# Kernel optimization log

Measured on AMD Instinct MI355X. Metric: run time of the kernel, lower is better.

Reference implementation:

```python
import jax, jax.numpy as jnp
import numpy as np

D_MODEL = 1024
NUM_HEADS = 16


def setup_inputs() -> dict:
    key = jax.random.key(0)
    ks = jax.random.split(key, 5)
    scale = 1.0 / np.sqrt(D_MODEL)
    X = jax.random.normal(ks[0], (4, 2048, D_MODEL), dtype=jnp.float32)
    W_q = jax.random.normal(ks[1], (D_MODEL, D_MODEL), dtype=jnp.float32) * scale
    W_k = jax.random.normal(ks[2], (D_MODEL, D_MODEL), dtype=jnp.float32) * scale
    W_v = jax.random.normal(ks[3], (D_MODEL, D_MODEL), dtype=jnp.float32) * scale
    W_o = jax.random.normal(ks[4], (D_MODEL, D_MODEL), dtype=jnp.float32) * scale
    return {"X": X, "W_q": W_q, "W_k": W_k, "W_v": W_v, "W_o": W_o}


def reference(X, W_q, W_k, W_v, W_o):
    b, s, d_model = X.shape
    h = NUM_HEADS
    d_k = d_model // h
    # Linear projections (y = x @ W^T convention; W stored as [out,in] would be
    # x @ W.T, but with random weights we use x @ W — math is identical in form).
    def split_heads(y):
        return y.reshape(b, s, h, d_k).transpose(0, 2, 1, 3)  # b h s d
    q = split_heads(X @ W_q)
    k = split_heads(X @ W_k)
    v = split_heads(X @ W_v)
    scores = jnp.einsum('bhid,bhjd->bhij', q, k) / jnp.sqrt(jnp.float32(d_k))
    causal = jnp.tril(jnp.ones((s, s), dtype=bool))
    scores = jnp.where(causal[None, None], scores, jnp.float32(-jnp.inf))
    probs = jax.nn.softmax(scores, axis=-1)
    attended = jnp.einsum('bhij,bhjd->bhid', probs, v)
    out = attended.transpose(0, 2, 1, 3).reshape(b, s, d_model)
    return out @ W_o
```

## Files before the change

kernel.cpp:

```cpp
#include <hip/hip_runtime.h>

typedef __bf16 bf16;
typedef __attribute__((ext_vector_type(8))) __bf16 bf16x8;
typedef __attribute__((ext_vector_type(4))) float f32x4;
typedef __attribute__((ext_vector_type(16))) float f32x16;
typedef __attribute__((ext_vector_type(4))) unsigned short u16x4;
typedef __attribute__((ext_vector_type(2))) int v2i;

#define D_MODEL 1024
#define SEQ     2048
#define NB      4
#define NH      16
#define DK      64
#define MROWS   (NB * SEQ)

#define MFMA_BF16 __builtin_amdgcn_mfma_f32_16x16x32_bf16
#define MFMA32    __builtin_amdgcn_mfma_f32_32x32x16_bf16
#define EXP2F(x) __builtin_amdgcn_exp2f(x)
#define QSCALE 0.18033688011112042f

__device__ __forceinline__ bf16 f2b(float f) {
    union { float f; unsigned u; } c; c.f = f;
    unsigned r = (c.u + 0x7fffu + ((c.u >> 16) & 1u)) >> 16;
    union { unsigned short s; bf16 b; } o; o.s = (unsigned short)r;
    return o.b;
}
__device__ __forceinline__ unsigned short f2u(float f) {
    union { float f; unsigned u; } c; c.f = f;
    return (unsigned short)((c.u + 0x7fffu + ((c.u >> 16) & 1u)) >> 16);
}

__device__ __forceinline__ f32x16 zero16() {
    f32x16 z = {0.f,0.f,0.f,0.f,0.f,0.f,0.f,0.f,
                0.f,0.f,0.f,0.f,0.f,0.f,0.f,0.f};
    return z;
}

template <int N> struct IC { static constexpr int v = N; };

__global__ void prep_kernel(const float* __restrict__ X,
                            const float* __restrict__ Wq, const float* __restrict__ Wk,
                            const float* __restrict__ Wv, const float* __restrict__ Wo,
                            bf16* __restrict__ Xb, bf16* __restrict__ WqkvT,
                            bf16* __restrict__ WoT) {
    __shared__ float tile[32][33];
    const int bid = blockIdx.x;
    if (bid < 8192) {
        int i = bid * 256 + threadIdx.x;
        float4 v = ((const float4*)X)[i];
        u16x4 o; o[0] = f2u(v.x); o[1] = f2u(v.y); o[2] = f2u(v.z); o[3] = f2u(v.w);
        ((u16x4*)Xb)[i] = o;
    } else {
        int r = bid - 8192;
        int w = r >> 10, tl = r & 1023;
        const float* src = (w == 0) ? Wq : (w == 1) ? Wk : (w == 2) ? Wv : Wo;
        bf16* dst = (w == 3) ? WoT : WqkvT + (size_t)w * 1024 * 1024;
        const int n0 = (tl & 31) * 32, k0 = (tl >> 5) * 32;
        const int tx = threadIdx.x & 31, ty = threadIdx.x >> 5;
#pragma unroll
        for (int i = 0; i < 4; i++)
            tile[ty + i * 8][tx] = src[(size_t)(k0 + ty + i * 8) * 1024 + n0 + tx];
        __syncthreads();
#pragma unroll
        for (int i = 0; i < 4; i++)
            dst[(size_t)(n0 + ty + i * 8) * 1024 + k0 + tx] = f2b(tile[tx][ty + i * 8]);
    }
}

__global__ __launch_bounds__(256) void gemm_qkv(const bf16* __restrict__ A,
                                                const bf16* __restrict__ Bt,
                                                bf16* __restrict__ outQ,
                                                bf16* __restrict__ outV) {
    __shared__ __align__(16) bf16 lA[128 * 64];
    __shared__ __align__(16) bf16 lB[128 * 64];

    const int t = threadIdx.x;
    const int wid = t >> 6, lane = t & 63;
    const int ln = lane & 15, qd = lane >> 4;
    const int wm = wid >> 1, wn = wid & 1;

    const int bid = blockIdx.x;
    const int idx = bid >> 3;
    const int colb = (bid & 7) * 3 + (idx % 3);
    const int rowb = idx / 3;
    const int row0 = rowb * 128, col0 = colb * 128;
    const bool isQK = (col0 < 2048);

    const int srow = t >> 3;
    const int schunk = (t & 7) ^ (srow & 7);
    const bf16* ga = A  + (size_t)(row0 + srow) * 1024 + schunk * 8;
    const bf16* gb = Bt + (size_t)(col0 + srow) * 1024 + schunk * 8;
    const int swk = ln & 7;

    f32x4 acc[4][4];
#pragma unroll
    for (int i = 0; i < 4; i++)
#pragma unroll
        for (int j = 0; j < 4; j++) acc[i][j] = (f32x4){0.f, 0.f, 0.f, 0.f};

    for (int kb = 0; kb < 1024; kb += 64) {
#pragma unroll
        for (int c = 0; c < 4; c++) {
            __builtin_amdgcn_global_load_lds(
                (const __attribute__((address_space(1))) void*)(ga + kb + (size_t)c * 32 * 1024),
                (__attribute__((address_space(3))) void*)(&lA[t * 8 + c * 2048]), 16, 0, 0);
            __builtin_amdgcn_global_load_lds(
                (const __attribute__((address_space(1))) void*)(gb + kb + (size_t)c * 32 * 1024),
                (__attribute__((address_space(3))) void*)(&lB[t * 8 + c * 2048]), 16, 0, 0);
        }
        __syncthreads();

#pragma unroll
        for (int ks = 0; ks < 2; ks++) {
            bf16x8 af[4], bfr[4];
#pragma unroll
            for (int i = 0; i < 4; i++)
                af[i] = *(const bf16x8*)&lA[(wm * 64 + i * 16 + ln) * 64
                                            + ((ks * 4 + qd) ^ swk) * 8];
#pragma unroll
            for (int j = 0; j < 4; j++)
                bfr[j] = *(const bf16x8*)&lB[(wn * 64 + j * 16 + ln) * 64
                                             + ((ks * 4 + qd) ^ swk) * 8];
            if (isQK) {
#pragma unroll
                for (int i = 0; i < 4; i++)
#pragma unroll
                    for (int j = 0; j < 4; j++)
                        acc[i][j] = MFMA_BF16(bfr[j], af[i], acc[i][j], 0, 0, 0);
            } else {
#pragma unroll
                for (int i = 0; i < 4; i++)
#pragma unroll
                    for (int j = 0; j < 4; j++)
                        acc[i][j] = MFMA_BF16(af[i], bfr[j], acc[i][j], 0, 0, 0);
            }
        }
        __syncthreads();
    }

    if (isQK) {
#pragma unroll
        for (int i = 0; i < 4; i++)
#pragma unroll
            for (int j = 0; j < 4; j++) {
                int m  = row0 + wm * 64 + i * 16 + ln;
                int n0 = col0 + wn * 64 + j * 16 + qd * 4;
                float scale = (n0 < 1024) ? QSCALE : 1.0f;
                int b = m >> 11, s = m & 2047;
                int h = (n0 & 1023) >> 6, d0 = n0 & 63;
                size_t addr = (((size_t)(b * NH + h) * SEQ + s) * DK + d0)
                              + (size_t)(n0 >> 10) * 8388608;
                u16x4 w;
#pragma unroll
                for (int r = 0; r < 4; r++) w[r] = f2u(acc[i][j][r] * scale);
                *(u16x4*)&outQ[addr] = w;
            }
    } else {
#pragma unroll
        for (int i = 0; i < 4; i++)
#pragma unroll
            for (int j = 0; j < 4; j++) {
                int m0 = row0 + wm * 64 + i * 16 + qd * 4;
                int n  = col0 + wn * 64 + j * 16 + ln - 2048;
                int b = m0 >> 11, s0 = m0 & 2047;
                int h = n >> 6, d = n & 63;
                size_t addr = ((size_t)(b * NH + h) * DK + d) * SEQ + s0;
                u16x4 w;
#pragma unroll
                for (int r = 0; r < 4; r++) w[r] = f2u(acc[i][j][r]);
                *(u16x4*)&outV[addr] = w;
            }
    }
}

__global__ __launch_bounds__(256) void gemm_o(const bf16* __restrict__ A,
                                              const bf16* __restrict__ Bt,
                                              float* __restrict__ out) {
    __shared__ __align__(16) bf16 lA[128 * 64];
    __shared__ __align__(16) bf16 lB[128 * 64];

    const int t = threadIdx.x;
    const int wid = t >> 6, lane = t & 63;
    const int ln = lane & 15, qd = lane >> 4;
    const int wm = wid >> 1, wn = wid & 1;

    const int bid = blockIdx.x;
    const int colb = bid & 7, rowb = bid >> 3;
    const int row0 = rowb * 128, col0 = colb * 128;

    const int srow = t >> 3;
    const int schunk = (t & 7) ^ (srow & 7);
    const bf16* ga = A  + (size_t)(row0 + srow) * 1024 + schunk * 8;
    const bf16* gb = Bt + (size_t)(col0 + srow) * 1024 + schunk * 8;
    const int swk = ln & 7;

    f32x4 acc[4][4];
#pragma unroll
    for (int i = 0; i < 4; i++)
#pragma unroll
        for (int j = 0; j < 4; j++) acc[i][j] = (f32x4){0.f, 0.f, 0.f, 0.f};

    for (int kb = 0; kb < 1024; kb += 64) {
#pragma unroll
        for (int c = 0; c < 4; c++) {
            __builtin_amdgcn_global_load_lds(
                (const __attribute__((address_space(1))) void*)(ga + kb + (size_t)c * 32 * 1024),
                (__attribute__((address_space(3))) void*)(&lA[t * 8 + c * 2048]), 16, 0, 0);
            __builtin_amdgcn_global_load_lds(
                (const __attribute__((address_space(1))) void*)(gb + kb + (size_t)c * 32 * 1024),
                (__attribute__((address_space(3))) void*)(&lB[t * 8 + c * 2048]), 16, 0, 0);
        }
        __syncthreads();

#pragma unroll
        for (int ks = 0; ks < 2; ks++) {
            bf16x8 af[4], bfr[4];
#pragma unroll
            for (int i = 0; i < 4; i++)
                af[i] = *(const bf16x8*)&lA[(wm * 64 + i * 16 + ln) * 64
                                            + ((ks * 4 + qd) ^ swk) * 8];
#pragma unroll
            for (int j = 0; j < 4; j++)
                bfr[j] = *(const bf16x8*)&lB[(wn * 64 + j * 16 + ln) * 64
                                             + ((ks * 4 + qd) ^ swk) * 8];
#pragma unroll
            for (int i = 0; i < 4; i++)
#pragma unroll
                for (int j = 0; j < 4; j++)
                    acc[i][j] = MFMA_BF16(bfr[j], af[i], acc[i][j], 0, 0, 0);
        }
        __syncthreads();
    }

#pragma unroll
    for (int i = 0; i < 4; i++)
#pragma unroll
        for (int j = 0; j < 4; j++) {
            int m  = row0 + wm * 64 + i * 16 + ln;
            int n0 = col0 + wn * 64 + j * 16 + qd * 4;
            *(f32x4*)&out[(size_t)m * 1024 + n0] = acc[i][j];
        }
}

__global__ __launch_bounds__(256, 3) void attn_kernel(const bf16* __restrict__ Q,
                                                      const bf16* __restrict__ K,
                                                      const bf16* __restrict__ Vt,
                                                      bf16* __restrict__ attn_out) {
    __shared__ __align__(16) bf16 smem[4][64 * 64];

    const int t = threadIdx.x;
    const int wid = t >> 6, lane = t & 63;
    const int qcol = lane & 31, h = lane >> 5;

    const int bid = blockIdx.x;
    const int bh = ((bid >> 7) << 3) | (bid & 7);
    const int g  = 15 - ((bid >> 3) & 15);
    const int nsteps = 2 * g + 2;

    const bf16* Qh = Q  + (size_t)bh * SEQ * DK;
    const bf16* Kh = K  + (size_t)bh * SEQ * DK;
    const bf16* Vh = Vt + (size_t)bh * DK * SEQ;

    const int qw0 = g * 128 + wid * 32;

    const int srow = t >> 3;
    const int schunk = (t & 7) ^ (srow & 7);
    const bf16* kgp = Kh + (size_t)srow * DK + schunk * 8;
    const bf16* vgp = Vh + (size_t)srow * SEQ + schunk * 8;

    const char* sbase = (const char*)&smem[0][0];
    int raddr[4];
#pragma unroll
    for (int tt = 0; tt < 4; tt++)
        raddr[tt] = qcol * 128 + (((2 * tt + h) ^ (lane & 7)) * 16);

    bf16x8 qf[4];
#pragma unroll
    for (int tt = 0; tt < 4; tt++)
        qf[tt] = *(const bf16x8*)(Qh + (size_t)(qw0 + qcol) * DK + tt * 16 + h * 8);

    f32x16 o[2];
    o[0] = zero16(); o[1] = zero16();
    float l = 0.f;

    auto stage = [&](int kb, int buf) {
#pragma unroll
        for (int c = 0; c < 2; c++) {
            __builtin_amdgcn_global_load_lds(
                (const __attribute__((address_space(1))) void*)(kgp + (size_t)(kb + c * 32) * DK),
                (__attribute__((address_space(3))) void*)(&smem[buf][t * 8 + c * 2048]), 16, 0, 0);
            __builtin_amdgcn_global_load_lds(
                (const __attribute__((address_space(1))) void*)(vgp + (size_t)c * 32 * SEQ + kb),
                (__attribute__((address_space(3))) void*)(&smem[2 + buf][t * 8 + c * 2048]), 16, 0, 0);
        }
    };

    auto step = [&](auto curc, int i) {
        constexpr int CUR = decltype(curc)::v;
        __syncthreads();
        const int nx = i + 1;
        if (nx < nsteps) stage(nx * 64, CUR ^ 1);
        const int kb = i * 64;
        const int nt = min(2, max(0, ((qw0 + 31 - kb) >> 5) + 1));
        if (nt > 0) {
            f32x16 st[2];
            __builtin_amdgcn_s_setprio(1);
#pragma unroll
            for (int n = 0; n < 2; n++)
                if (n < nt) {
                    f32x16 z = zero16();
#pragma unroll
                    for (int tt = 0; tt < 4; tt++) {
                        bf16x8 kf = *(const bf16x8*)(sbase + raddr[tt]
                                        + (CUR * 8192 + n * 4096));
                        z = MFMA32(kf, qf[tt], z, 0, 0, 0);
                    }
                    st[n] = z;
                }
            __builtin_amdgcn_s_setprio(0);

            float ps = 0.f;
#pragma unroll
            for (int n = 0; n < 2; n++)
                if (n < nt) {
                    const bool diag = (kb + 32 * n == qw0);
#pragma unroll
                    for (int r = 0; r < 16; r++) {
                        float pv = EXP2F(st[n][r]);
                        if (diag) {
                            const int kloc = (r & 3) + 8 * (r >> 2) + 4 * h;
                            pv = (kloc > qcol) ? 0.f : pv;
                        }
                        st[n][r] = pv;
                    }
                    float s0 = (st[n][0] + st[n][1]) + (st[n][2] + st[n][3]);
                    float s1 = (st[n][4] + st[n][5]) + (st[n][6] + st[n][7]);
                    float s2 = (st[n][8] + st[n][9]) + (st[n][10] + st[n][11]);
                    float s3 = (st[n][12] + st[n][13]) + (st[n][14] + st[n][15]);
                    ps += (s0 + s1) + (s2 + s3);
                }
            l += ps;

#pragma unroll
            for (int ks = 0; ks < 4; ks++)
                if (ks < 2 * nt) {
                    const int n = ks >> 1, b8 = (ks & 1) * 8;
                    unsigned A, B, C, D;
                    asm("v_cvt_pk_bf16_f32 %0, %1, %2"
                        : "=v"(A) : "v"(st[n][b8 + 0]), "v"(st[n][b8 + 1]));
                    asm("v_cvt_pk_bf16_f32 %0, %1, %2"
                        : "=v"(B) : "v"(st[n][b8 + 2]), "v"(st[n][b8 + 3]));
                    asm("v_cvt_pk_bf16_f32 %0, %1, %2"
                        : "=v"(C) : "v"(st[n][b8 + 4]), "v"(st[n][b8 + 5]));
                    asm("v_cvt_pk_bf16_f32 %0, %1, %2"
                        : "=v"(D) : "v"(st[n][b8 + 6]), "v"(st[n][b8 + 7]));
                    v2i r02 = __builtin_amdgcn_permlane32_swap((int)A, (int)C, false, false);
                    v2i r13 = __builtin_amdgcn_permlane32_swap((int)B, (int)D, false, false);
                    union { unsigned u[4]; bf16x8 v; } pf;
                    pf.u[0] = (unsigned)r02[0];
                    pf.u[1] = (unsigned)r13[0];
                    pf.u[2] = (unsigned)r02[1];
                    pf.u[3] = (unsigned)r13[1];
                    __builtin_amdgcn_s_setprio(1);
#pragma unroll
                    for (int m = 0; m < 2; m++) {
                        bf16x8 vf = *(const bf16x8*)(sbase + raddr[ks]
                                        + (16384 + CUR * 8192 + m * 4096));
                        o[m] = MFMA32(vf, pf.v, o[m], 0, 0, 0);
                    }
                    __builtin_amdgcn_s_setprio(0);
                }
        }
    };

    stage(0, 0);
    step(IC<0>{}, 0);
    for (int ii = 0; ii < g; ii++) {
        step(IC<1>{}, 2 * ii + 1);
        step(IC<0>{}, 2 * ii + 2);
    }
    step(IC<1>{}, 2 * g + 1);

    l += __shfl_xor(l, 32);
    const float inv = 1.0f / l;
    const int b = bh >> 4, head = bh & 15;
    const size_t orow = ((size_t)(b * SEQ + qw0 + qcol)) * D_MODEL + head * DK;
#pragma unroll
    for (int m = 0; m < 2; m++)
#pragma unroll
        for (int q4 = 0; q4 < 4; q4++) {
            u16x4 w;
#pragma unroll
            for (int c = 0; c < 4; c++) w[c] = f2u(o[m][q4 * 4 + c] * inv);
            *(u16x4*)&attn_out[orow + m * 32 + q4 * 8 + h * 4] = w;
        }
}

extern "C" void kernel_launch(void* const* d_in, const int* in_sizes, int n_in,
                              void* d_out, int out_size, void* d_ws, size_t ws_size,
                              hipStream_t stream) {
    const float* X  = (const float*)d_in[0];
    const float* Wq = (const float*)d_in[1];
    const float* Wk = (const float*)d_in[2];
    const float* Wv = (const float*)d_in[3];
    const float* Wo = (const float*)d_in[4];
    float* out = (float*)d_out;
    char* ws = (char*)d_ws;

    bf16* Xb    = (bf16*)(ws);
    bf16* WqkvT = (bf16*)(ws + (16u << 20));
    bf16* WoT   = (bf16*)(ws + (22u << 20));
    bf16* Qb    = (bf16*)(ws + (24u << 20));
    bf16* Vt    = (bf16*)(ws + (56u << 20));
    bf16* Attn  = Xb;
    bf16* Kb    = Qb + (size_t)8388608;

    prep_kernel<<<dim3(12288), dim3(256), 0, stream>>>(X, Wq, Wk, Wv, Wo,
                                                       Xb, WqkvT, WoT);

    gemm_qkv<<<dim3(1536), dim3(256), 0, stream>>>(Xb, WqkvT, Qb, Vt);

    attn_kernel<<<dim3(1024), dim3(256), 0, stream>>>(Qb, Kb, Vt, Attn);

    gemm_o<<<dim3(512), dim3(256), 0, stream>>>(Attn, WoT, out);
}
```

Before: 257.2 us.

## Pair complementary causal query blocks per workgroup for balanced attention work

After: 240.5 us, median of 2. 1.07x faster.

```diff
diff --git a/kernel.cpp b/kernel.cpp
--- a/kernel.cpp
+++ b/kernel.cpp
@@ -242,7 +242,7 @@
         }
 }
 
-__global__ __launch_bounds__(256, 3) void attn_kernel(const bf16* __restrict__ Q,
+__global__ __launch_bounds__(128, 2) void attn_kernel(const bf16* __restrict__ Q,
                                                       const bf16* __restrict__ K,
                                                       const bf16* __restrict__ Vt,
                                                       bf16* __restrict__ attn_out) {
@@ -254,14 +254,13 @@
 
     const int bid = blockIdx.x;
     const int bh = ((bid >> 7) << 3) | (bid & 7);
-    const int g  = 15 - ((bid >> 3) & 15);
-    const int nsteps = 2 * g + 2;
+    const int p  = (bid >> 3) & 15;
+    const int gA = 31 - p, gB = p;
+    const int ntA = gA + 1;
 
     const bf16* Qh = Q  + (size_t)bh * SEQ * DK;
     const bf16* Kh = K  + (size_t)bh * SEQ * DK;
     const bf16* Vh = Vt + (size_t)bh * DK * SEQ;
-
-    const int qw0 = g * 128 + wid * 32;
 
     const int srow = t >> 3;
     const int schunk = (t & 7) ^ (srow & 7);
@@ -274,56 +273,124 @@
     for (int tt = 0; tt < 4; tt++)
         raddr[tt] = qcol * 128 + (((2 * tt + h) ^ (lane & 7)) * 16);
 
+    int qw0;
     bf16x8 qf[4];
-#pragma unroll
-    for (int tt = 0; tt < 4; tt++)
-        qf[tt] = *(const bf16x8*)(Qh + (size_t)(qw0 + qcol) * DK + tt * 16 + h * 8);
-
     f32x16 o[2];
-    o[0] = zero16(); o[1] = zero16();
-    float l = 0.f;
+    float l;
+
+    auto initGroup = [&](int g) {
+        qw0 = g * 64 + wid * 32;
+#pragma unroll
+        for (int tt = 0; tt < 4; tt++)
+            qf[tt] = *(const bf16x8*)(Qh + (size_t)(qw0 + qcol) * DK + tt * 16 + h * 8);
+        o[0] = zero16(); o[1] = zero16();
+        l = 0.f;
+    };
+
+    const int b = bh >> 4, head = bh & 15;
+    auto finalize = [&]() {
+        float ll = l + __shfl_xor(l, 32);
+        const float inv = 1.0f / ll;
+        const size_t orow = ((size_t)(b * SEQ + qw0 + qcol)) * D_MODEL + head * DK;
+#pragma unroll
+        for (int m = 0; m < 2; m++)
+#pragma unroll
+            for (int q4 = 0; q4 < 4; q4++) {
+                u16x4 w;
+#pragma unroll
+                for (int c = 0; c < 4; c++) w[c] = f2u(o[m][q4 * 4 + c] * inv);
+                *(u16x4*)&attn_out[orow + m * 32 + q4 * 8 + h * 4] = w;
+            }
+    };
 
     auto stage = [&](int kb, int buf) {
 #pragma unroll
-        for (int c = 0; c < 2; c++) {
-            __builtin_amdgcn_global_load_lds(
-                (const __attribute__((address_space(1))) void*)(kgp + (size_t)(kb + c * 32) * DK),
-                (__attribute__((address_space(3))) void*)(&smem[buf][t * 8 + c * 2048]), 16, 0, 0);
-            __builtin_amdgcn_global_load_lds(
-                (const __attribute__((address_space(1))) void*)(vgp + (size_t)c * 32 * SEQ + kb),
-                (__attribute__((address_space(3))) void*)(&smem[2 + buf][t * 8 + c * 2048]), 16, 0, 0);
-        }
-    };
-
-    auto step = [&](auto curc, int i) {
+        for (int c = 0; c < 4; c++) {
+            __builtin_amdgcn_global_load_lds(
+                (const __attribute__((address_space(1))) void*)(kgp + (size_t)(kb + c * 16) * DK),
+                (__attribute__((address_space(3))) void*)(&smem[buf][t * 8 + c * 1024]), 16, 0, 0);
+            __builtin_amdgcn_global_load_lds(
+                (const __attribute__((address_space(1))) void*)(vgp + (size_t)c * 16 * SEQ + kb),
+                (__attribute__((address_space(3))) void*)(&smem[2 + buf][t * 8 + c * 1024]), 16, 0, 0);
+        }
+    };
+
+    auto qkt = [&](const char* kb_base) -> f32x16 {
+        f32x16 z = zero16();
+#pragma unroll
+        for (int tt = 0; tt < 4; tt++) {
+            bf16x8 kf = *(const bf16x8*)(kb_base + raddr[tt]);
+            z = MFMA32(kf, qf[tt], z, 0, 0, 0);
+        }
+        return z;
+    };
+
+    auto pvks = [&](const f32x16& s, int b8, int ks, const char* vbase) {
+        unsigned A, B, C, D;
+        asm("v_cvt_pk_bf16_f32 %0, %1, %2"
+            : "=v"(A) : "v"(s[b8 + 0]), "v"(s[b8 + 1]));
+        asm("v_cvt_pk_bf16_f32 %0, %1, %2"
+            : "=v"(B) : "v"(s[b8 + 2]), "v"(s[b8 + 3]));
+        asm("v_cvt_pk_bf16_f32 %0, %1, %2"
+            : "=v"(C) : "v"(s[b8 + 4]), "v"(s[b8 + 5]));
+        asm("v_cvt_pk_bf16_f32 %0, %1, %2"
+            : "=v"(D) : "v"(s[b8 + 6]), "v"(s[b8 + 7]));
+        v2i r02 = __builtin_amdgcn_permlane32_swap((int)A, (int)C, false, false);
+        v2i r13 = __builtin_amdgcn_permlane32_swap((int)B, (int)D, false, false);
+        union { unsigned u[4]; bf16x8 v; } pf;
+        pf.u[0] = (unsigned)r02[0];
+        pf.u[1] = (unsigned)r13[0];
+        pf.u[2] = (unsigned)r02[1];
+        pf.u[3] = (unsigned)r13[1];
+#pragma unroll
+        for (int m = 0; m < 2; m++) {
+            bf16x8 vf = *(const bf16x8*)(vbase + raddr[ks] + m * 4096);
+            o[m] = MFMA32(vf, pf.v, o[m], 0, 0, 0);
+        }
+    };
+
+    auto smaxFull = [&](f32x16& s) -> float {
+#pragma unroll
+        for (int r = 0; r < 16; r++) s[r] = EXP2F(s[r]);
+        float s0 = (s[0] + s[1]) + (s[2] + s[3]);
+        float s1 = (s[4] + s[5]) + (s[6] + s[7]);
+        float s2 = (s[8] + s[9]) + (s[10] + s[11]);
+        float s3 = (s[12] + s[13]) + (s[14] + s[15]);
+        return (s0 + s1) + (s2 + s3);
+    };
+
+    auto compute = [&](auto curc, int kb) {
         constexpr int CUR = decltype(curc)::v;
-        __syncthreads();
-        const int nx = i + 1;
-        if (nx < nsteps) stage(nx * 64, CUR ^ 1);
-        const int kb = i * 64;
-        const int nt = min(2, max(0, ((qw0 + 31 - kb) >> 5) + 1));
-        if (nt > 0) {
+        const char* kbase = sbase + CUR * 8192;
+        const char* vbase = sbase + 16384 + CUR * 8192;
+        const int rel = qw0 - kb;
+        if (rel < 0) return;
+        if (rel >= 64) {
+            __builtin_amdgcn_s_setprio(1);
+            f32x16 s0 = qkt(kbase);
+            f32x16 s1 = qkt(kbase + 4096);
+            __builtin_amdgcn_s_setprio(0);
+            l += smaxFull(s0);
+            __builtin_amdgcn_s_setprio(1);
+            pvks(s0, 0, 0, vbase);
+            pvks(s0, 8, 1, vbase);
+            __builtin_amdgcn_s_setprio(0);
+            l += smaxFull(s1);
+            __builtin_amdgcn_s_setprio(1);
+            pvks(s1, 0, 2, vbase);
+            pvks(s1, 8, 3, vbase);
+            __builtin_amdgcn_s_setprio(0);
+        } else {
+            const int nt = (rel >> 5) + 1;
             f32x16 st[2];
-            __builtin_amdgcn_s_setprio(1);
+#pragma unroll
+            for (int n = 0; n < 2; n++)
+                if (n < nt) st[n] = qkt(kbase + n * 4096);
+            float ps = 0.f;
 #pragma unroll
             for (int n = 0; n < 2; n++)
                 if (n < nt) {
-                    f32x16 z = zero16();
-#pragma unroll
-                    for (int tt = 0; tt < 4; tt++) {
-                        bf16x8 kf = *(const bf16x8*)(sbase + raddr[tt]
-                                        + (CUR * 8192 + n * 4096));
-                        z = MFMA32(kf, qf[tt], z, 0, 0, 0);
-                    }
-                    st[n] = z;
-                }
-            __builtin_amdgcn_s_setprio(0);
-
-            float ps = 0.f;
-#pragma unroll
-            for (int n = 0; n < 2; n++)
-                if (n < nt) {
-                    const bool diag = (kb + 32 * n == qw0);
+                    const bool diag = (rel == 32 * n);
 #pragma unroll
                     for (int r = 0; r < 16; r++) {
                         float pv = EXP2F(st[n][r]);
@@ -340,60 +407,36 @@
                     ps += (s0 + s1) + (s2 + s3);
                 }
             l += ps;
-
 #pragma unroll
             for (int ks = 0; ks < 4; ks++)
-                if (ks < 2 * nt) {
-                    const int n = ks >> 1, b8 = (ks & 1) * 8;
-                    unsigned A, B, C, D;
-                    asm("v_cvt_pk_bf16_f32 %0, %1, %2"
-                        : "=v"(A) : "v"(st[n][b8 + 0]), "v"(st[n][b8 + 1]));
-                    asm("v_cvt_pk_bf16_f32 %0, %1, %2"
-                        : "=v"(B) : "v"(st[n][b8 + 2]), "v"(st[n][b8 + 3]));
-                    asm("v_cvt_pk_bf16_f32 %0, %1, %2"
-                        : "=v"(C) : "v"(st[n][b8 + 4]), "v"(st[n][b8 + 5]));
-                    asm("v_cvt_pk_bf16_f32 %0, %1, %2"
-                        : "=v"(D) : "v"(st[n][b8 + 6]), "v"(st[n][b8 + 7]));
-                    v2i r02 = __builtin_amdgcn_permlane32_swap((int)A, (int)C, false, false);
-                    v2i r13 = __builtin_amdgcn_permlane32_swap((int)B, (int)D, false, false);
-                    union { unsigned u[4]; bf16x8 v; } pf;
-                    pf.u[0] = (unsigned)r02[0];
-                    pf.u[1] = (unsigned)r13[0];
-                    pf.u[2] = (unsigned)r02[1];
-                    pf.u[3] = (unsigned)r13[1];
-                    __builtin_amdgcn_s_setprio(1);
-#pragma unroll
-                    for (int m = 0; m < 2; m++) {
-                        bf16x8 vf = *(const bf16x8*)(sbase + raddr[ks]
-                                        + (16384 + CUR * 8192 + m * 4096));
-                        o[m] = MFMA32(vf, pf.v, o[m], 0, 0, 0);
-                    }
-                    __builtin_amdgcn_s_setprio(0);
-                }
-        }
+                if (ks < 2 * nt)
+                    pvks(st[ks >> 1], (ks & 1) * 8, ks, vbase);
+        }
+    };
+
+    auto step = [&](auto curc, int i) {
+        constexpr int CUR = decltype(curc)::v;
+        __syncthreads();
+        const int nx = i + 1;
+        if (nx < 33) {
+            const int tnx = (nx < ntA) ? nx : nx - ntA;
+            stage(tnx * 64, CUR ^ 1);
+        }
+        const int kb = ((i < ntA) ? i : i - ntA) * 64;
+        compute(curc, kb);
+        if (i == ntA - 1) { finalize(); initGroup(gB); }
     };
 
     stage(0, 0);
+    initGroup(gA);
+
     step(IC<0>{}, 0);
-    for (int ii = 0; ii < g; ii++) {
+#pragma unroll 1
+    for (int ii = 0; ii < 16; ii++) {
         step(IC<1>{}, 2 * ii + 1);
         step(IC<0>{}, 2 * ii + 2);
     }
-    step(IC<1>{}, 2 * g + 1);
-
-    l += __shfl_xor(l, 32);
-    const float inv = 1.0f / l;
-    const int b = bh >> 4, head = bh & 15;
-    const size_t orow = ((size_t)(b * SEQ + qw0 + qcol)) * D_MODEL + head * DK;
-#pragma unroll
-    for (int m = 0; m < 2; m++)
-#pragma unroll
-        for (int q4 = 0; q4 < 4; q4++) {
-            u16x4 w;
-#pragma unroll
-            for (int c = 0; c < 4; c++) w[c] = f2u(o[m][q4 * 4 + c] * inv);
-            *(u16x4*)&attn_out[orow + m * 32 + q4 * 8 + h * 4] = w;
-        }
+    finalize();
 }
 
 extern "C" void kernel_launch(void* const* d_in, const int* in_sizes, int n_in,
@@ -420,7 +463,7 @@
 
     gemm_qkv<<<dim3(1536), dim3(256), 0, stream>>>(Xb, WqkvT, Qb, Vt);
 
-    attn_kernel<<<dim3(1024), dim3(256), 0, stream>>>(Qb, Kb, Vt, Attn);
+    attn_kernel<<<dim3(1024), dim3(128), 0, stream>>>(Qb, Kb, Vt, Attn);
 
     gemm_o<<<dim3(512), dim3(256), 0, stream>>>(Attn, WoT, out);
 }
```
